# Kernel tuning notes

Hardware: AMD Instinct MI355X
Metric: run time of the kernel (lower is better)

Reference implementation:

```python
import jax, jax.numpy as jnp
import numpy as np

B, V, T, K, N = 2048, 256, 11, 8, 8
H = 2 ** N - 1  # 255 combination neurons per slot


def setup_inputs() -> dict:
    key = jax.random.key(0)
    k0, k1, k2, k3, k4 = jax.random.split(key, 5)
    # one-hot character ids, matching make_scanner_batch semantics: (B, V, T, K)
    ids = jax.random.randint(k0, (B, T, K), 0, V)
    x_unfolded = jax.nn.one_hot(ids, V, axis=1, dtype=jnp.float32)
    # scanner_w ~ U(-1/sqrt(V), 1/sqrt(V)), shape (N, V, K)
    bv = 1.0 / np.sqrt(V).astype(np.float32)
    scanner_w = jax.random.uniform(k1, (N, V, K), jnp.float32, -bv, bv)
    # grouped 1x1 conv: torch weight (K*H, N, 1) -> store (K*H, N); fan_in = N
    bh = 1.0 / np.sqrt(N).astype(np.float32)
    hidden_w = jax.random.uniform(k2, (K * H, N), jnp.float32, -bh, bh)
    # output 1x1 conv: (2, K*H, 1) -> (2, K*H); fan_in = K*H
    bo = 1.0 / np.sqrt(K * H).astype(np.float32)
    out_w = jax.random.uniform(k3, (2, K * H), jnp.float32, -bo, bo)
    out_b = jax.random.uniform(k4, (2,), jnp.float32, -bo, bo)
    return {"x_unfolded": x_unfolded, "scanner_w": scanner_w,
            "hidden_w": hidden_w, "out_w": out_w, "out_b": out_b}


def reference(x_unfolded, scanner_w, hidden_w, out_w, out_b):
    # x_unfolded: (B, V, T, K); scanner_w: (N, V, K)
    b, v, t, k = x_unfolded.shape
    n = scanner_w.shape[0]
    h_per_slot = hidden_w.shape[0] // k
    # one-hot matmul (equivalent to a gather): result (B, K, N, T),
    # i.e. channel order after reshape is slot-major (k*N + n), matching
    # torch's permute(0,3,1,2).reshape(B, K*N, T).
    h = jax.nn.relu(jnp.einsum('bvtk,nvk->bknt', x_unfolded, scanner_w))
    # grouped 1x1 conv with groups=K: group k maps its N scanner values to
    # h_per_slot neurons. torch weight (K*H, N, 1) -> (K, H, N), where output
    # channel o belongs to group o // H.
    hw = hidden_w.reshape(k, h_per_slot, n)
    h2 = jax.nn.relu(jnp.einsum('bknt,khn->bkht', h, hw)).reshape(b, k * h_per_slot, t)
    # final 1x1 conv with bias: (B, 2, T)
    return jnp.einsum('bct,oc->bot', h2, out_w) + out_b[None, :, None]
```

## Files before the change

### kernel.cpp

```cpp
#include <hip/hip_runtime.h>

constexpr int B_ = 2048;
constexpr int V_ = 256;
constexpr int T_ = 11;
constexpr int K_ = 8;
constexpr int N_ = 8;
constexpr int H_ = 255;
constexpr int TK = T_ * K_;
constexpr int XB = V_ * TK;
constexpr int SLAB = 92;

__global__ __launch_bounds__(256, 4)
void scan_ids(const float* __restrict__ x,
              int* __restrict__ ids)
{
    const int tid = threadIdx.x;
    const int b   = blockIdx.x;
    const uint4* xb = (const uint4*)(x + (size_t)b * XB);
    int* __restrict__ idb = ids + b * TK;

    #pragma unroll
    for (int c = 0; c < 3; ++c) {
        const int nload = (c < 2) ? 8 : 6;
        uint4 vbuf[8];
        #pragma unroll
        for (int i = 0; i < 8; ++i)
            if (i < nload) vbuf[i] = xb[(c * 8 + i) * 256 + tid];
        #pragma unroll
        for (int i = 0; i < 8; ++i) {
            if (i < nload) {
                const uint4 q = vbuf[i];
                if (q.x | q.y | q.z | q.w) {
                    const int F = ((c * 8 + i) * 256 + tid) * 4;
                    if (q.x) { const int f = F;     const int v = f / TK; idb[f - v * TK] = v; }
                    if (q.y) { const int f = F + 1; const int v = f / TK; idb[f - v * TK] = v; }
                    if (q.z) { const int f = F + 2; const int v = f / TK; idb[f - v * TK] = v; }
                    if (q.w) { const int f = F + 3; const int v = f / TK; idb[f - v * TK] = v; }
                }
            }
        }
    }
}

__global__ __launch_bounds__(256, 3)
void scanner_mlp(const int* __restrict__ ids,
                 const float* __restrict__ sw,
                 const float* __restrict__ hw,
                 const float* __restrict__ ow,
                 const float* __restrict__ ob,
                 float* __restrict__ out)
{
    __shared__ int   ids_sh[TK];
    __shared__ float hsh[K_ * SLAB];
    __shared__ float wred[4][22];

    const int tid = threadIdx.x;
    const int b   = blockIdx.x;

    if (tid < TK) ids_sh[tid] = ids[b * TK + tid];
    __syncthreads();

    #pragma unroll
    for (int j = 0; j < 3; ++j) {
        const int idx = j * 256 + tid;
        if (idx < TK * N_) {
            const int entry = idx >> 3;
            const int n     = idx & 7;
            const int t     = entry >> 3;
            const int k     = entry & 7;
            const int v     = ids_sh[entry];
            hsh[k * SLAB + t * 8 + n] = fmaxf(sw[(n * V_ + v) * K_ + k], 0.0f);
        }
    }
    __syncthreads();

    const int k2 = tid >> 5;
    const int hb = tid & 31;

    float hreg[T_][N_];
    #pragma unroll
    for (int t = 0; t < T_; ++t) {
        const float4* p = (const float4*)(hsh + k2 * SLAB + t * 8);
        const float4 a0 = p[0];
        const float4 a1 = p[1];
        hreg[t][0] = a0.x; hreg[t][1] = a0.y; hreg[t][2] = a0.z; hreg[t][3] = a0.w;
        hreg[t][4] = a1.x; hreg[t][5] = a1.y; hreg[t][6] = a1.z; hreg[t][7] = a1.w;
    }

    float acc0[T_], acc1[T_];
    #pragma unroll
    for (int t = 0; t < T_; ++t) { acc0[t] = 0.0f; acc1[t] = 0.0f; }

    #pragma unroll
    for (int i = 0; i < 8; ++i) {
        const int hh = hb + 32 * i;
        if (hh < H_) {
            const int row = k2 * H_ + hh;
            const float4* hwp = (const float4*)(hw + row * 8);
            const float4 w0 = hwp[0];
            const float4 w1 = hwp[1];
            const float o0 = ow[row];
            const float o1 = ow[K_ * H_ + row];
            #pragma unroll
            for (int t = 0; t < T_; ++t) {
                float pre = w0.x * hreg[t][0];
                pre = fmaf(w0.y, hreg[t][1], pre);
                pre = fmaf(w0.z, hreg[t][2], pre);
                pre = fmaf(w0.w, hreg[t][3], pre);
                pre = fmaf(w1.x, hreg[t][4], pre);
                pre = fmaf(w1.y, hreg[t][5], pre);
                pre = fmaf(w1.z, hreg[t][6], pre);
                pre = fmaf(w1.w, hreg[t][7], pre);
                const float h2 = fmaxf(pre, 0.0f);
                acc0[t] = fmaf(h2, o0, acc0[t]);
                acc1[t] = fmaf(h2, o1, acc1[t]);
            }
        }
    }

    #pragma unroll
    for (int t = 0; t < T_; ++t) {
        #pragma unroll
        for (int off = 32; off >= 1; off >>= 1) {
            acc0[t] += __shfl_xor(acc0[t], off, 64);
            acc1[t] += __shfl_xor(acc1[t], off, 64);
        }
    }
    const int wave = tid >> 6;
    const int lane = tid & 63;
    if (lane == 0) {
        #pragma unroll
        for (int t = 0; t < T_; ++t) {
            wred[wave][t]      = acc0[t];
            wred[wave][11 + t] = acc1[t];
        }
    }
    __syncthreads();

    if (tid < 22) {
        const float s = wred[0][tid] + wred[1][tid] + wred[2][tid] + wred[3][tid];
        out[(size_t)b * 22 + tid] = s + ob[tid / 11];
    }
}

extern "C" void kernel_launch(void* const* d_in, const int* in_sizes, int n_in,
                              void* d_out, int out_size, void* d_ws, size_t ws_size,
                              hipStream_t stream) {
    const float* x  = (const float*)d_in[0];
    const float* sw = (const float*)d_in[1];
    const float* hw = (const float*)d_in[2];
    const float* ow = (const float*)d_in[3];
    const float* ob = (const float*)d_in[4];
    float* out = (float*)d_out;

    int* ids = (int*)d_ws;

    scan_ids<<<B_, 256, 0, stream>>>(x, ids);
    scanner_mlp<<<B_, 256, 0, stream>>>(ids, sw, hw, ow, ob, out);
}
```

Baseline: 282.8 us.

## Precompute per-slot vocab lookup table and fuse scan with table lookup

```diff
diff --git a/kernel.cpp b/kernel.cpp
--- a/kernel.cpp
+++ b/kernel.cpp
@@ -6,18 +6,71 @@
 constexpr int K_ = 8;
 constexpr int N_ = 8;
 constexpr int H_ = 255;
+constexpr int KH_ = K_ * H_;
 constexpr int TK = T_ * K_;
 constexpr int XB = V_ * TK;
-constexpr int SLAB = 92;
+
+
+__global__ __launch_bounds__(256)
+void build_lut(const float* __restrict__ sw,
+               const float* __restrict__ hw,
+               const float* __restrict__ ow,
+               float2* __restrict__ G2)
+{
+    const int g    = blockIdx.x * 256 + threadIdx.x;
+    const int pair = g >> 2;
+    const int q    = g & 3;
+    const int k    = pair >> 8;
+    const int v    = pair & 255;
+
+    float sv[N_];
+    #pragma unroll
+    for (int n = 0; n < N_; ++n)
+        sv[n] = fmaxf(sw[(n * V_ + v) * K_ + k], 0.0f);
+
+    float a0 = 0.0f, a1 = 0.0f;
+    const int hbase = q * 64;
+    #pragma unroll 8
+    for (int j = 0; j < 64; ++j) {
+        const int h = hbase + j;
+        if (h < H_) {
+            const int row = k * H_ + h;
+            const float4* hp = (const float4*)(hw + row * 8);
+            const float4 w0 = hp[0];
+            const float4 w1 = hp[1];
+            float pre = w0.x * sv[0];
+            pre = fmaf(w0.y, sv[1], pre);
+            pre = fmaf(w0.z, sv[2], pre);
+            pre = fmaf(w0.w, sv[3], pre);
+            pre = fmaf(w1.x, sv[4], pre);
+            pre = fmaf(w1.y, sv[5], pre);
+            pre = fmaf(w1.z, sv[6], pre);
+            pre = fmaf(w1.w, sv[7], pre);
+            const float h2 = fmaxf(pre, 0.0f);
+            a0 = fmaf(h2, ow[row], a0);
+            a1 = fmaf(h2, ow[KH_ + row], a1);
+        }
+    }
+    a0 += __shfl_xor(a0, 1, 64);
+    a0 += __shfl_xor(a0, 2, 64);
+    a1 += __shfl_xor(a1, 1, 64);
+    a1 += __shfl_xor(a1, 2, 64);
+    if (q == 0) G2[pair] = make_float2(a0, a1);
+}
 
 __global__ __launch_bounds__(256, 4)
-void scan_ids(const float* __restrict__ x,
-              int* __restrict__ ids)
+void scan_lookup(const float* __restrict__ x,
+                 const float2* __restrict__ G2,
+                 const float* __restrict__ ob,
+                 float* __restrict__ out)
 {
+    __shared__ int   ids_sh[TK];
+    __shared__ float g0[TK];
+    __shared__ float g1[TK];
+
     const int tid = threadIdx.x;
     const int b   = blockIdx.x;
     const uint4* xb = (const uint4*)(x + (size_t)b * XB);
-    int* __restrict__ idb = ids + b * TK;
 
     #pragma unroll
     for (int c = 0; c < 3; ++c) {
@@ -32,114 +85,31 @@
                 const uint4 q = vbuf[i];
                 if (q.x | q.y | q.z | q.w) {
                     const int F = ((c * 8 + i) * 256 + tid) * 4;
-                    if (q.x) { const int f = F;     const int v = f / TK; idb[f - v * TK] = v; }
-                    if (q.y) { const int f = F + 1; const int v = f / TK; idb[f - v * TK] = v; }
-                    if (q.z) { const int f = F + 2; const int v = f / TK; idb[f - v * TK] = v; }
-                    if (q.w) { const int f = F + 3; const int v = f / TK; idb[f - v * TK] = v; }
+                    if (q.x) { const int f = F;     const int v = f / TK; ids_sh[f - v * TK] = v; }
+                    if (q.y) { const int f = F + 1; const int v = f / TK; ids_sh[f - v * TK] = v; }
+                    if (q.z) { const int f = F + 2; const int v = f / TK; ids_sh[f - v * TK] = v; }
+                    if (q.w) { const int f = F + 3; const int v = f / TK; ids_sh[f - v * TK] = v; }
                 }
             }
         }
     }
-}
-
-__global__ __launch_bounds__(256, 3)
-void scanner_mlp(const int* __restrict__ ids,
-                 const float* __restrict__ sw,
-                 const float* __restrict__ hw,
-                 const float* __restrict__ ow,
-                 const float* __restrict__ ob,
-                 float* __restrict__ out)
-{
-    __shared__ int   ids_sh[TK];
-    __shared__ float hsh[K_ * SLAB];
-    __shared__ float wred[4][22];
-
-    const int tid = threadIdx.x;
-    const int b   = blockIdx.x;
-
-    if (tid < TK) ids_sh[tid] = ids[b * TK + tid];
     __syncthreads();
 
-    #pragma unroll
-    for (int j = 0; j < 3; ++j) {
-        const int idx = j * 256 + tid;
-        if (idx < TK * N_) {
-            const int entry = idx >> 3;
-            const int n     = idx & 7;
-            const int t     = entry >> 3;
-            const int k     = entry & 7;
-            const int v     = ids_sh[entry];
-            hsh[k * SLAB + t * 8 + n] = fmaxf(sw[(n * V_ + v) * K_ + k], 0.0f);
-        }
-    }
-    __syncthreads();
-
-    const int k2 = tid >> 5;
-    const int hb = tid & 31;
-
-    float hreg[T_][N_];
-    #pragma unroll
-    for (int t = 0; t < T_; ++t) {
-        const float4* p = (const float4*)(hsh + k2 * SLAB + t * 8);
-        const float4 a0 = p[0];
-        const float4 a1 = p[1];
-        hreg[t][0] = a0.x; hreg[t][1] = a0.y; hreg[t][2] = a0.z; hreg[t][3] = a0.w;
-        hreg[t][4] = a1.x; hreg[t][5] = a1.y; hreg[t][6] = a1.z; hreg[t][7] = a1.w;
-    }
-
-    float acc0[T_], acc1[T_];
-    #pragma unroll
-    for (int t = 0; t < T_; ++t) { acc0[t] = 0.0f; acc1[t] = 0.0f; }
-
-    #pragma unroll
-    for (int i = 0; i < 8; ++i) {
-        const int hh = hb + 32 * i;
-        if (hh < H_) {
-            const int row = k2 * H_ + hh;
-            const float4* hwp = (const float4*)(hw + row * 8);
-            const float4 w0 = hwp[0];
-            const float4 w1 = hwp[1];
-            const float o0 = ow[row];
-            const float o1 = ow[K_ * H_ + row];
-            #pragma unroll
-            for (int t = 0; t < T_; ++t) {
-                float pre = w0.x * hreg[t][0];
-                pre = fmaf(w0.y, hreg[t][1], pre);
-                pre = fmaf(w0.z, hreg[t][2], pre);
-                pre = fmaf(w0.w, hreg[t][3], pre);
-                pre = fmaf(w1.x, hreg[t][4], pre);
-                pre = fmaf(w1.y, hreg[t][5], pre);
-                pre = fmaf(w1.z, hreg[t][6], pre);
-                pre = fmaf(w1.w, hreg[t][7], pre);
-                const float h2 = fmaxf(pre, 0.0f);
-                acc0[t] = fmaf(h2, o0, acc0[t]);
-                acc1[t] = fmaf(h2, o1, acc1[t]);
-            }
-        }
-    }
-
-    #pragma unroll
-    for (int t = 0; t < T_; ++t) {
-        #pragma unroll
-        for (int off = 32; off >= 1; off >>= 1) {
-            acc0[t] += __shfl_xor(acc0[t], off, 64);
-            acc1[t] += __shfl_xor(acc1[t], off, 64);
-        }
-    }
-    const int wave = tid >> 6;
-    const int lane = tid & 63;
-    if (lane == 0) {
-        #pragma unroll
-        for (int t = 0; t < T_; ++t) {
-            wred[wave][t]      = acc0[t];
-            wred[wave][11 + t] = acc1[t];
-        }
+    if (tid < TK) {
+        const int k = tid & 7;
+        const float2 gg = G2[k * V_ + ids_sh[tid]];
+        g0[tid] = gg.x;
+        g1[tid] = gg.y;
     }
     __syncthreads();
 
     if (tid < 22) {
-        const float s = wred[0][tid] + wred[1][tid] + wred[2][tid] + wred[3][tid];
-        out[(size_t)b * 22 + tid] = s + ob[tid / 11];
+        const int o = tid / 11;
+        const int t = tid - o * 11;
+        const float* gp = (o ? g1 : g0) + t * 8;
+        const float s = ((gp[0] + gp[1]) + (gp[2] + gp[3]))
+                      + ((gp[4] + gp[5]) + (gp[6] + gp[7]));
+        out[(size_t)b * 22 + tid] = s + ob[o];
     }
 }
 
@@ -153,8 +123,8 @@
     const float* ob = (const float*)d_in[4];
     float* out = (float*)d_out;
 
-    int* ids = (int*)d_ws;
+    float2* G2 = (float2*)d_ws;
 
-    scan_ids<<<B_, 256, 0, stream>>>(x, ids);
-    scanner_mlp<<<B_, 256, 0, stream>>>(ids, sw, hw, ow, ob, out);
+    build_lut<<<32, 256, 0, stream>>>(sw, hw, ow, G2);
+    scan_lookup<<<B_, 256, 0, stream>>>(x, G2, ob, out);
 }
```

Result: no change. 278.3 us (-1.6%).
